# Performance work log

Measured on AMD Instinct MI355X. Metric: run time of the kernel, lower is better.

The kernel has to match this reference:

```python
import jax, jax.numpy as jnp
import numpy as np

NUM_FILTERS = 512
NUM_HEADS = 8
D_HEAD = NUM_FILTERS // NUM_HEADS


def setup_inputs() -> dict:
    key = jax.random.key(0)
    ks = jax.random.split(key, 11)
    B, W, H, F = 4, 48, 48, NUM_FILTERS
    s = 1.0 / np.sqrt(F)
    return {
        "query": jax.random.normal(ks[0], (B, W, H, F), jnp.float32),
        "value": jax.random.normal(ks[1], (B, W, H, F), jnp.float32),
        "keys": jax.random.normal(ks[2], (B, W, H, F), jnp.float32),
        "wq_w": jax.random.normal(ks[3], (F, F), jnp.float32) * s,
        "wq_b": jnp.zeros((F,), jnp.float32),
        "wk_w": jax.random.normal(ks[4], (F, F), jnp.float32) * s,
        "wk_b": jnp.zeros((F,), jnp.float32),
        "wv_w": jax.random.normal(ks[5], (F, F), jnp.float32) * s,
        "wv_b": jnp.zeros((F,), jnp.float32),
        "wo_w": jax.random.normal(ks[6], (F, F), jnp.float32) * s,
        "wo_b": jnp.zeros((F,), jnp.float32),
    }


def reference(query, value, keys, wq_w, wq_b, wk_w, wk_b, wv_w, wv_b, wo_w, wo_b):
    B, W, H, F = query.shape
    h, d = NUM_HEADS, D_HEAD
    # flatten spatial -> sequence, project, split heads: [B, h, S, d]
    def proj(x, w, b):
        x = x.reshape(B, -1, F) @ w + b
        return x.reshape(B, -1, h, d).transpose(0, 2, 1, 3)
    q = proj(query, wq_w, wq_b)
    k = proj(keys, wk_w, wk_b)
    v = proj(value, wv_w, wv_b)
    # scaled dot-product attention (mask=None path)
    logits = jnp.einsum('bhqd,bhkd->bhqk', q, k) / jnp.sqrt(jnp.asarray(d, q.dtype))
    attn = jax.nn.softmax(logits, axis=-1)            # [B, h, S, S]
    ctx = jnp.einsum('bhqk,bhkd->bhqd', attn, v)      # [B, h, S, d]
    ctx = ctx.transpose(0, 2, 1, 3).reshape(B, -1, F)  # [B, S, F]
    out = (ctx @ wo_w + wo_b).reshape(B, W, H, F)
    attn_weights = attn.reshape(B, h, W, H, -1)        # [B, h, W, H, S]
    return out, attn_weights
```

## Files before the change

kernel.cpp:

```cpp
#include <hip/hip_runtime.h>
#include <cstddef>

#define BB 4
#define SS 2304
#define FF 512
#define NH 8
#define DD 64
#define BSR (BB*SS)

typedef __attribute__((ext_vector_type(8))) short bf16x8;
typedef __attribute__((ext_vector_type(4))) float f32x4;
#define MFMA16(a,b,c) __builtin_amdgcn_mfma_f32_16x16x32_bf16((a),(b),(c),0,0,0)

__device__ __forceinline__ ushort f2bf_rne(float x) {
    uint u = __float_as_uint(x);
    uint r = u + 0x7fffu + ((u >> 16) & 1u);
    return (ushort)(r >> 16);
}
__device__ __forceinline__ float bfval(ushort h) {
    return __uint_as_float((uint)h << 16);
}

__global__ __launch_bounds__(256) void wtsplit_all(
    const float* __restrict__ w0, const float* __restrict__ w1,
    const float* __restrict__ w2, const float* __restrict__ w3,
    ushort* __restrict__ whi_all, ushort* __restrict__ wlo_all)
{
    __shared__ __align__(16) float tile[64][68];
    const int z = blockIdx.z;
    const float* w = (z == 0) ? w0 : (z == 1) ? w1 : (z == 2) ? w2 : w3;
    ushort* whi = whi_all + (size_t)z * FF * FF;
    ushort* wlo = wlo_all + (size_t)z * FF * FF;

    const int t  = threadIdx.x;
    const int kt = blockIdx.x;
    const int nt = blockIdx.y;
    {
        const int r  = t >> 2;
        const int cg = (t & 3) * 16;
        const float* src = w + (size_t)(kt * 64 + r) * FF + nt * 64 + cg;
        #pragma unroll
        for (int j = 0; j < 4; ++j)
            *(float4*)&tile[r][cg + 4 * j] = *(const float4*)(src + 4 * j);
    }
    __syncthreads();
    {
        const int n  = t >> 2;
        const int kg = (t & 3) * 16;
        union { ushort s[16]; uint4 q[2]; } H, L;
        #pragma unroll
        for (int j = 0; j < 16; ++j) {
            float x = tile[kg + j][n];
            ushort hh = f2bf_rne(x);
            H.s[j] = hh;
            L.s[j] = f2bf_rne(x - bfval(hh));
        }
        size_t off = (size_t)(nt * 64 + n) * FF + kt * 64 + kg;
        *(uint4*)(whi + off)     = H.q[0];
        *(uint4*)(whi + off + 8) = H.q[1];
        *(uint4*)(wlo + off)     = L.q[0];
        *(uint4*)(wlo + off + 8) = L.q[1];
    }
}

__global__ __launch_bounds__(256) void vtsplit_kernel(
    const float* __restrict__ v, ushort* __restrict__ vthi)
{
    __shared__ __align__(16) float tile[64][68];
    const int t  = threadIdx.x;
    const int st = blockIdx.x;
    const int bh = blockIdx.y;
    {
        const int r  = t >> 2;
        const int cg = (t & 3) * 16;
        const float* src = v + ((size_t)bh * SS + st * 64 + r) * DD + cg;
        #pragma unroll
        for (int j = 0; j < 4; ++j)
            *(float4*)&tile[r][cg + 4 * j] = *(const float4*)(src + 4 * j);
    }
    __syncthreads();
    {
        const int d  = t >> 2;
        const int sg = (t & 3) * 16;
        union { ushort s[16]; uint4 q[2]; } H;
        #pragma unroll
        for (int j = 0; j < 16; ++j) H.s[j] = f2bf_rne(tile[sg + j][d]);
        size_t off = ((size_t)bh * DD + d) * SS + st * 64 + sg;
        *(uint4*)(vthi + off)     = H.q[0];
        *(uint4*)(vthi + off + 8) = H.q[1];
    }
}

__global__ __launch_bounds__(256) void proj_qkv(
    const float* __restrict__ q_in, const float* __restrict__ k_in,
    const float* __restrict__ v_in, const ushort* __restrict__ whi_all,
    const ushort* __restrict__ wlo_all, const float* __restrict__ bq,
    const float* __restrict__ bk, const float* __restrict__ bv,
    ushort* __restrict__ qhi, ushort* __restrict__ qlo,
    ushort* __restrict__ khi, ushort* __restrict__ klo,
    float* __restrict__ vstage)
{
    const int z = blockIdx.z;
    const float* X = (z == 0) ? q_in : (z == 1) ? k_in : v_in;
    const ushort* wth = whi_all + (size_t)z * FF * FF;
    const ushort* wtl = wlo_all + (size_t)z * FF * FF;
    const float* bias = (z == 0) ? bq : (z == 1) ? bk : bv;

    const int t  = threadIdx.x, w = t >> 6, l = t & 63;
    const int ar = l & 15, kg = (l >> 4) * 8;
    const int i0 = blockIdx.x * 64, j0 = blockIdx.y * 128;
    const int arow = i0 + w * 16 + ar;

    f32x4 acc[8];
    #pragma unroll
    for (int nt = 0; nt < 8; ++nt) acc[nt] = (f32x4){0.f, 0.f, 0.f, 0.f};

    for (int kk = 0; kk < FF; kk += 32) {
        const float* xr = X + (size_t)arow * FF + kk + kg;
        float4 f0 = *(const float4*)xr;
        float4 f1 = *(const float4*)(xr + 4);
        ushort h0 = f2bf_rne(f0.x), h1 = f2bf_rne(f0.y), h2 = f2bf_rne(f0.z), h3 = f2bf_rne(f0.w);
        ushort h4 = f2bf_rne(f1.x), h5 = f2bf_rne(f1.y), h6 = f2bf_rne(f1.z), h7 = f2bf_rne(f1.w);
        union { uint u[4]; bf16x8 v; } ah, al;
        ah.u[0] = (uint)h0 | ((uint)h1 << 16);
        ah.u[1] = (uint)h2 | ((uint)h3 << 16);
        ah.u[2] = (uint)h4 | ((uint)h5 << 16);
        ah.u[3] = (uint)h6 | ((uint)h7 << 16);
        if (z < 2) {
            al.u[0] = (uint)f2bf_rne(f0.x - bfval(h0)) | ((uint)f2bf_rne(f0.y - bfval(h1)) << 16);
            al.u[1] = (uint)f2bf_rne(f0.z - bfval(h2)) | ((uint)f2bf_rne(f0.w - bfval(h3)) << 16);
            al.u[2] = (uint)f2bf_rne(f1.x - bfval(h4)) | ((uint)f2bf_rne(f1.y - bfval(h5)) << 16);
            al.u[3] = (uint)f2bf_rne(f1.z - bfval(h6)) | ((uint)f2bf_rne(f1.w - bfval(h7)) << 16);
        }
        #pragma unroll
        for (int nt = 0; nt < 8; ++nt) {
            const size_t wo = (size_t)(j0 + nt * 16 + ar) * FF + kk + kg;
            bf16x8 bh = *(const bf16x8*)(wth + wo);
            bf16x8 bl = *(const bf16x8*)(wtl + wo);
            acc[nt] = MFMA16(ah.v, bh, acc[nt]);
            acc[nt] = MFMA16(ah.v, bl, acc[nt]);
            if (z < 2) acc[nt] = MFMA16(al.v, bh, acc[nt]);
        }
    }

    const int bidx = i0 / SS;
    ushort* ohi = (z == 0) ? qhi : khi;
    ushort* olo = (z == 0) ? qlo : klo;
    #pragma unroll
    for (int nt = 0; nt < 8; ++nt) {
        const int col = j0 + nt * 16 + ar;
        const float bb = bias[col];
        #pragma unroll
        for (int r = 0; r < 4; ++r) {
            const int rowl = w * 16 + (l >> 4) * 4 + r;
            const float val = acc[nt][r] + bb;
            const int s = (i0 - bidx * SS) + rowl;
            const size_t o = (((size_t)bidx * NH + (col >> 6)) * SS + s) * DD + (col & 63);
            if (z == 2) {
                vstage[o] = val;
            } else {
                ushort hv = f2bf_rne(val);
                ohi[o] = hv;
                olo[o] = f2bf_rne(val - bfval(hv));
            }
        }
    }
}

__global__ __launch_bounds__(256) void proj_out(
    const float* __restrict__ X, const ushort* __restrict__ wth,
    const ushort* __restrict__ wtl, const float* __restrict__ bias,
    float* __restrict__ outf)
{
    const int t  = threadIdx.x, w = t >> 6, l = t & 63;
    const int ar = l & 15, kg = (l >> 4) * 8;
    const int i0 = blockIdx.x * 64, j0 = blockIdx.y * 128;
    const int arow = i0 + w * 16 + ar;

    f32x4 acc[8];
    #pragma unroll
    for (int nt = 0; nt < 8; ++nt) acc[nt] = (f32x4){0.f, 0.f, 0.f, 0.f};

    for (int kk = 0; kk < FF; kk += 32) {
        const float* xr = X + (size_t)arow * FF + kk + kg;
        float4 f0 = *(const float4*)xr;
        float4 f1 = *(const float4*)(xr + 4);
        union { uint u[4]; bf16x8 v; } ah;
        ah.u[0] = (uint)f2bf_rne(f0.x) | ((uint)f2bf_rne(f0.y) << 16);
        ah.u[1] = (uint)f2bf_rne(f0.z) | ((uint)f2bf_rne(f0.w) << 16);
        ah.u[2] = (uint)f2bf_rne(f1.x) | ((uint)f2bf_rne(f1.y) << 16);
        ah.u[3] = (uint)f2bf_rne(f1.z) | ((uint)f2bf_rne(f1.w) << 16);
        #pragma unroll
        for (int nt = 0; nt < 8; ++nt) {
            const size_t wo = (size_t)(j0 + nt * 16 + ar) * FF + kk + kg;
            bf16x8 bh = *(const bf16x8*)(wth + wo);
            bf16x8 bl = *(const bf16x8*)(wtl + wo);
            acc[nt] = MFMA16(ah.v, bh, acc[nt]);
            acc[nt] = MFMA16(ah.v, bl, acc[nt]);
        }
    }

    #pragma unroll
    for (int nt = 0; nt < 8; ++nt) {
        const int col = j0 + nt * 16 + ar;
        const float bb = bias[col];
        #pragma unroll
        for (int r = 0; r < 4; ++r) {
            const int rowl = w * 16 + (l >> 4) * 4 + r;
            outf[(size_t)(i0 + rowl) * FF + col] = acc[nt][r] + bb;
        }
    }
}

__global__ __launch_bounds__(512, 4) void fattn_kernel(
    const ushort* __restrict__ qhi, const ushort* __restrict__ qlo,
    const ushort* __restrict__ khi, const ushort* __restrict__ klo,
    const ushort* __restrict__ vthi,
    float* __restrict__ attn_out, float* __restrict__ ctx)
{
    __shared__ __align__(16) unsigned char smem[67584];
    ushort* KH0 = (ushort*)smem;
    ushort* KH1 = KH0 + 4096;
    ushort* KL0 = KH1 + 4096;
    ushort* KL1 = KL0 + 4096;
    ushort* VH0 = KL1 + 4096;
    ushort* VH1 = VH0 + 4096;
    float*  PT  = (float*)(VH1 + 4096);
    float*  redS = PT;

    const int t = threadIdx.x, w = t >> 6, l = t & 63;
    const int ar = l & 15, kgi = l >> 4;
    const int kg = kgi * 8;
    const int qs = w & 3, kh = w >> 2;

    const int xcd = blockIdx.x & 7;
    const int pos = blockIdx.x >> 3;
    const int bh  = xcd * 4 + (pos / 36);
    const int qt  = pos % 36;
    const int q0  = qt * 64;
    const int b   = bh >> 3, h = bh & 7;
    const size_t base = (size_t)bh * SS * DD;
    const float SC = 0.125f * 1.44269504f;

    const size_t qo = base + (size_t)(q0 + qs * 16 + ar) * DD + kg;
    const bf16x8 qh0 = *(const bf16x8*)(qhi + qo);
    const bf16x8 qh1 = *(const bf16x8*)(qhi + qo + 32);
    const bf16x8 ql0 = *(const bf16x8*)(qlo + qo);
    const bf16x8 ql1 = *(const bf16x8*)(qlo + qo + 32);

    const int srow = t >> 3, sc8 = t & 7;
    const int sidx = srow * 64 + ((sc8 ^ (srow & 7)) << 3);
    const ushort* khsrc = khi + base + srow * 64 + sc8 * 8;
    const ushort* klsrc = klo + base + srow * 64 + sc8 * 8;
    const ushort* vhsrc = vthi + ((size_t)bh * DD + srow) * SS + sc8 * 8;

    const int sw  = ar & 7;
    const int i00 = kh * 2048 + ar * 64;
    const int i01 = i00 + 1024;
    const int s00 = (kgi ^ sw) << 3;
    const int s01 = ((4 | kgi) ^ sw) << 3;
    const int svw = ((kh * 4 + kgi) ^ sw) << 3;

    float s_[4] = {0.f, 0.f, 0.f, 0.f};
    {
        uint4 rk = *(const uint4*)khsrc;
        *(uint4*)&KH0[sidx] = rk;
        __syncthreads();
        for (int kt = 0; kt < 36; ++kt) {
            if (kt < 35) rk = *(const uint4*)(khsrc + (size_t)(kt + 1) * 4096);
            const ushort* KC = (kt & 1) ? KH1 : KH0;
            bf16x8 b00 = *(const bf16x8*)&KC[i00 + s00];
            bf16x8 b01 = *(const bf16x8*)&KC[i00 + s01];
            bf16x8 b10 = *(const bf16x8*)&KC[i01 + s00];
            bf16x8 b11 = *(const bf16x8*)&KC[i01 + s01];
            f32x4 a0 = {0.f,0.f,0.f,0.f}, a1 = {0.f,0.f,0.f,0.f};
            __builtin_amdgcn_s_setprio(1);
            a0 = MFMA16(qh0, b00, a0); a1 = MFMA16(qh0, b10, a1);
            a0 = MFMA16(qh1, b01, a0); a1 = MFMA16(qh1, b11, a1);
            __builtin_amdgcn_s_setprio(0);
            #pragma unroll
            for (int r = 0; r < 4; ++r)
                s_[r] += exp2f(a0[r] * SC) + exp2f(a1[r] * SC);
            if (kt < 35) {
                ushort* KN = (kt & 1) ? KH0 : KH1;
                *(uint4*)&KN[sidx] = rk;
            }
            __syncthreads();
        }
    }
    #pragma unroll
    for (int off = 1; off <= 8; off <<= 1) {
        #pragma unroll
        for (int r = 0; r < 4; ++r) s_[r] += __shfl_xor(s_[r], off);
    }
    if (ar == 0) {
        #pragma unroll
        for (int r = 0; r < 4; ++r)
            redS[kh * 64 + qs * 16 + kgi * 4 + r] = s_[r];
    }
    __syncthreads();
    float inv[4];
    #pragma unroll
    for (int r = 0; r < 4; ++r) {
        const int idx = qs * 16 + kgi * 4 + r;
        inv[r] = 1.0f / (redS[idx] + redS[64 + idx]);
    }

    float* PTw = PT + w * 576;
    float* asto = attn_out + ((size_t)bh * SS + q0 + qs * 16 + (l >> 2)) * SS
                + kh * 32 + (l & 3) * 8;

    f32x4 acc[4];
    #pragma unroll
    for (int nt = 0; nt < 4; ++nt) acc[nt] = (f32x4){0.f, 0.f, 0.f, 0.f};

    {
        uint4 a = *(const uint4*)khsrc;
        uint4 bq = *(const uint4*)klsrc;
        uint4 c = *(const uint4*)vhsrc;
        *(uint4*)&KH0[sidx] = a;
        *(uint4*)&KL0[sidx] = bq;
        *(uint4*)&VH0[sidx] = c;
    }
    __syncthreads();

    for (int kt = 0; kt < 36; ++kt) {
        uint4 rkh, rkl, rvh;
        if (kt < 35) {
            rkh = *(const uint4*)(khsrc + (size_t)(kt + 1) * 4096);
            rkl = *(const uint4*)(klsrc + (size_t)(kt + 1) * 4096);
            rvh = *(const uint4*)(vhsrc + (size_t)(kt + 1) * 64);
        }
        const ushort* KHc = (kt & 1) ? KH1 : KH0;
        const ushort* KLc = (kt & 1) ? KL1 : KL0;
        const ushort* VHc = (kt & 1) ? VH1 : VH0;

        bf16x8 bh00 = *(const bf16x8*)&KHc[i00 + s00];
        bf16x8 bh01 = *(const bf16x8*)&KHc[i00 + s01];
        bf16x8 bl00 = *(const bf16x8*)&KLc[i00 + s00];
        bf16x8 bl01 = *(const bf16x8*)&KLc[i00 + s01];
        bf16x8 bh10 = *(const bf16x8*)&KHc[i01 + s00];
        bf16x8 bh11 = *(const bf16x8*)&KHc[i01 + s01];
        bf16x8 bl10 = *(const bf16x8*)&KLc[i01 + s00];
        bf16x8 bl11 = *(const bf16x8*)&KLc[i01 + s01];
        f32x4 a0 = {0.f,0.f,0.f,0.f}, a1 = {0.f,0.f,0.f,0.f};
        __builtin_amdgcn_s_setprio(1);
        a0 = MFMA16(qh0, bh00, a0); a1 = MFMA16(qh0, bh10, a1);
        a0 = MFMA16(qh0, bl00, a0); a1 = MFMA16(qh0, bl10, a1);
        a0 = MFMA16(ql0, bh00, a0); a1 = MFMA16(ql0, bh10, a1);
        a0 = MFMA16(qh1, bh01, a0); a1 = MFMA16(qh1, bh11, a1);
        a0 = MFMA16(qh1, bl01, a0); a1 = MFMA16(qh1, bl11, a1);
        a0 = MFMA16(ql1, bh01, a0); a1 = MFMA16(ql1, bh11, a1);
        __builtin_amdgcn_s_setprio(0);

        #pragma unroll
        for (int r = 0; r < 4; ++r) {
            const int row = kgi * 4 + r;
            float p0 = exp2f(a0[r] * SC) * inv[r];
            float p1 = exp2f(a1[r] * SC) * inv[r];
            PTw[row * 36 + ar]      = p0;
            PTw[row * 36 + 16 + ar] = p1;
        }

        {
            const float* psr = PTw + (l >> 2) * 36 + (l & 3) * 8;
            f32x4 sv0 = *(const f32x4*)psr;
            f32x4 sv1 = *(const f32x4*)(psr + 4);
            f32x4* dst = (f32x4*)(asto + (size_t)kt * 64);
            __builtin_nontemporal_store(sv0, dst);
            __builtin_nontemporal_store(sv1, dst + 1);
        }

        {
            const float* par = PTw + ar * 36 + kg;
            f32x4 pf0 = *(const f32x4*)par;
            f32x4 pf1 = *(const f32x4*)(par + 4);
            union { uint u[4]; bf16x8 v; } pah, pal;
            ushort hh[8]; float rr[8];
            #pragma unroll
            for (int j = 0; j < 4; ++j) {
                hh[j]     = f2bf_rne(pf0[j]); rr[j]     = pf0[j] - bfval(hh[j]);
                hh[4 + j] = f2bf_rne(pf1[j]); rr[4 + j] = pf1[j] - bfval(hh[4 + j]);
            }
            #pragma unroll
            for (int j = 0; j < 4; ++j) {
                pah.u[j] = (uint)hh[2*j] | ((uint)hh[2*j+1] << 16);
                pal.u[j] = (uint)f2bf_rne(rr[2*j]) | ((uint)f2bf_rne(rr[2*j+1]) << 16);
            }
            __builtin_amdgcn_s_setprio(1);
            #pragma unroll
            for (int nt = 0; nt < 4; ++nt) {
                const int vfi = (nt * 16 + ar) * 64 + svw;
                bf16x8 vh = *(const bf16x8*)&VHc[vfi];
                acc[nt] = MFMA16(pah.v, vh, acc[nt]);
                acc[nt] = MFMA16(pal.v, vh, acc[nt]);
            }
            __builtin_amdgcn_s_setprio(0);
        }

        if (kt < 35) {
            ushort* KHN = (kt & 1) ? KH0 : KH1;
            ushort* KLN = (kt & 1) ? KL0 : KL1;
            ushort* VHN = (kt & 1) ? VH0 : VH1;
            *(uint4*)&KHN[sidx] = rkh;
            *(uint4*)&KLN[sidx] = rkl;
            *(uint4*)&VHN[sidx] = rvh;
        }
        __syncthreads();
    }

    float* SCR = (float*)smem;
    #pragma unroll
    for (int nt = 0; nt < 4; ++nt) {
        #pragma unroll
        for (int r = 0; r < 4; ++r)
            SCR[w * 1088 + (kgi * 4 + r) * 68 + nt * 16 + ar] = acc[nt][r];
    }
    __syncthreads();
    {
        const int rrow = t >> 3;
        const int dg   = (t & 7) * 8;
        const int rqs  = rrow >> 4, rl = rrow & 15;
        const float* s0p = SCR + rqs * 1088 + rl * 68 + dg;
        const float* s1p = s0p + 4 * 1088;
        f32x4 o0, o1;
        #pragma unroll
        for (int j = 0; j < 4; ++j) o0[j] = s0p[j] + s1p[j];
        #pragma unroll
        for (int j = 0; j < 4; ++j) o1[j] = s0p[4 + j] + s1p[4 + j];
        float* cdst = ctx + ((size_t)b * SS + q0 + rrow) * FF + h * DD + dg;
        *(f32x4*)cdst = o0;
        *(f32x4*)(cdst + 4) = o1;
    }
}

extern "C" void kernel_launch(void* const* d_in, const int* in_sizes, int n_in,
                              void* d_out, int out_size, void* d_ws, size_t ws_size,
                              hipStream_t stream) {
    (void)in_sizes; (void)n_in; (void)out_size; (void)ws_size;
    const float* query = (const float*)d_in[0];
    const float* value = (const float*)d_in[1];
    const float* keys  = (const float*)d_in[2];
    const float* wq_w  = (const float*)d_in[3];
    const float* wq_b  = (const float*)d_in[4];
    const float* wk_w  = (const float*)d_in[5];
    const float* wk_b  = (const float*)d_in[6];
    const float* wv_w  = (const float*)d_in[7];
    const float* wv_b  = (const float*)d_in[8];
    const float* wo_w  = (const float*)d_in[9];
    const float* wo_b  = (const float*)d_in[10];

    float* out  = (float*)d_out;
    float* attn = out + (size_t)BB * SS * FF;

    const size_t NQ = (size_t)BB * NH * SS * DD;
    ushort* qhi    = (ushort*)d_ws;
    ushort* qlo    = qhi + NQ;
    ushort* khi    = qlo + NQ;
    ushort* klo    = khi + NQ;
    ushort* vthi   = klo + NQ;
    float*  vstage = (float*)(vthi + NQ);
    ushort* wthi   = (ushort*)(vstage + NQ);
    ushort* wtlo   = wthi + (size_t)4 * FF * FF;

    dim3 gwt(FF / 64, FF / 64, 4);
    dim3 gqkv(BSR / 64, FF / 128, 3);
    dim3 gproj(BSR / 64, FF / 128);
    dim3 gvt(SS / 64, BB * NH);

    wtsplit_all<<<gwt, 256, 0, stream>>>(wq_w, wk_w, wv_w, wo_w, wthi, wtlo);
    proj_qkv<<<gqkv, 256, 0, stream>>>(query, keys, value, wthi, wtlo,
                                       wq_b, wk_b, wv_b,
                                       qhi, qlo, khi, klo, vstage);
    vtsplit_kernel<<<gvt, 256, 0, stream>>>(vstage, vthi);

    fattn_kernel<<<36 * 32, 512, 0, stream>>>(qhi, qlo, khi, klo, vthi,
                                              attn, vstage);

    proj_out<<<gproj, 256, 0, stream>>>(vstage, wthi + (size_t)3 * FF * FF,
                                        wtlo + (size_t)3 * FF * FF, wo_b, out);
}
```

Baseline: 640.3 us.

## Fuse V transpose into projection epilogue and use packed bf16 conversions

Removes the separate vtsplit kernel by having proj_qkv write V already transposed to bf16 via a shared-memory tile. The Q/K epilogue is also staged through LDS so hi/lo outputs go out as coalesced 16-byte stores. Manual bf16 rounding is replaced by the hardware v_cvt_pk_bf16_f32 instruction throughout. The softmax normalisation is folded into the exp2 argument as a log-domain offset. Together these cut a kernel launch and an fp32 round trip, at the cost of extra LDS use and barriers in the projection epilogue.

New measurement: 603.4 us (median of 2 runs). 1.06x faster.

```diff
diff --git a/kernel.cpp b/kernel.cpp
--- a/kernel.cpp
+++ b/kernel.cpp
@@ -20,6 +20,13 @@
 __device__ __forceinline__ float bfval(ushort h) {
     return __uint_as_float((uint)h << 16);
 }
+__device__ __forceinline__ uint cvt_pk_bf16(float a, float b) {
+    uint r;
+    asm("v_cvt_pk_bf16_f32 %0, %1, %2" : "=v"(r) : "v"(a), "v"(b));
+    return r;
+}
+__device__ __forceinline__ float lo16val(uint p) { return __uint_as_float(p << 16); }
+__device__ __forceinline__ float hi16val(uint p) { return __uint_as_float(p & 0xffff0000u); }
 
 __global__ __launch_bounds__(256) void wtsplit_all(
     const float* __restrict__ w0, const float* __restrict__ w1,
@@ -47,47 +54,20 @@
     {
         const int n  = t >> 2;
         const int kg = (t & 3) * 16;
-        union { ushort s[16]; uint4 q[2]; } H, L;
-        #pragma unroll
-        for (int j = 0; j < 16; ++j) {
-            float x = tile[kg + j][n];
-            ushort hh = f2bf_rne(x);
-            H.s[j] = hh;
-            L.s[j] = f2bf_rne(x - bfval(hh));
+        uint H[8], L[8];
+        #pragma unroll
+        for (int j = 0; j < 8; ++j) {
+            float x0 = tile[kg + 2 * j][n];
+            float x1 = tile[kg + 2 * j + 1][n];
+            uint hp = cvt_pk_bf16(x0, x1);
+            H[j] = hp;
+            L[j] = cvt_pk_bf16(x0 - lo16val(hp), x1 - hi16val(hp));
         }
         size_t off = (size_t)(nt * 64 + n) * FF + kt * 64 + kg;
-        *(uint4*)(whi + off)     = H.q[0];
-        *(uint4*)(whi + off + 8) = H.q[1];
-        *(uint4*)(wlo + off)     = L.q[0];
-        *(uint4*)(wlo + off + 8) = L.q[1];
-    }
-}
-
-__global__ __launch_bounds__(256) void vtsplit_kernel(
-    const float* __restrict__ v, ushort* __restrict__ vthi)
-{
-    __shared__ __align__(16) float tile[64][68];
-    const int t  = threadIdx.x;
-    const int st = blockIdx.x;
-    const int bh = blockIdx.y;
-    {
-        const int r  = t >> 2;
-        const int cg = (t & 3) * 16;
-        const float* src = v + ((size_t)bh * SS + st * 64 + r) * DD + cg;
-        #pragma unroll
-        for (int j = 0; j < 4; ++j)
-            *(float4*)&tile[r][cg + 4 * j] = *(const float4*)(src + 4 * j);
-    }
-    __syncthreads();
-    {
-        const int d  = t >> 2;
-        const int sg = (t & 3) * 16;
-        union { ushort s[16]; uint4 q[2]; } H;
-        #pragma unroll
-        for (int j = 0; j < 16; ++j) H.s[j] = f2bf_rne(tile[sg + j][d]);
-        size_t off = ((size_t)bh * DD + d) * SS + st * 64 + sg;
-        *(uint4*)(vthi + off)     = H.q[0];
-        *(uint4*)(vthi + off + 8) = H.q[1];
+        *(uint4*)(whi + off)     = make_uint4(H[0], H[1], H[2], H[3]);
+        *(uint4*)(whi + off + 8) = make_uint4(H[4], H[5], H[6], H[7]);
+        *(uint4*)(wlo + off)     = make_uint4(L[0], L[1], L[2], L[3]);
+        *(uint4*)(wlo + off + 8) = make_uint4(L[4], L[5], L[6], L[7]);
     }
 }
 
@@ -98,8 +78,10 @@
     const float* __restrict__ bk, const float* __restrict__ bv,
     ushort* __restrict__ qhi, ushort* __restrict__ qlo,
     ushort* __restrict__ khi, ushort* __restrict__ klo,
-    float* __restrict__ vstage)
+    ushort* __restrict__ vthi)
 {
+    __shared__ __align__(16) ushort TL[9216];
+
     const int z = blockIdx.z;
     const float* X = (z == 0) ? q_in : (z == 1) ? k_in : v_in;
     const ushort* wth = whi_all + (size_t)z * FF * FF;
@@ -119,18 +101,16 @@
         const float* xr = X + (size_t)arow * FF + kk + kg;
         float4 f0 = *(const float4*)xr;
         float4 f1 = *(const float4*)(xr + 4);
-        ushort h0 = f2bf_rne(f0.x), h1 = f2bf_rne(f0.y), h2 = f2bf_rne(f0.z), h3 = f2bf_rne(f0.w);
-        ushort h4 = f2bf_rne(f1.x), h5 = f2bf_rne(f1.y), h6 = f2bf_rne(f1.z), h7 = f2bf_rne(f1.w);
         union { uint u[4]; bf16x8 v; } ah, al;
-        ah.u[0] = (uint)h0 | ((uint)h1 << 16);
-        ah.u[1] = (uint)h2 | ((uint)h3 << 16);
-        ah.u[2] = (uint)h4 | ((uint)h5 << 16);
-        ah.u[3] = (uint)h6 | ((uint)h7 << 16);
+        ah.u[0] = cvt_pk_bf16(f0.x, f0.y);
+        ah.u[1] = cvt_pk_bf16(f0.z, f0.w);
+        ah.u[2] = cvt_pk_bf16(f1.x, f1.y);
+        ah.u[3] = cvt_pk_bf16(f1.z, f1.w);
         if (z < 2) {
-            al.u[0] = (uint)f2bf_rne(f0.x - bfval(h0)) | ((uint)f2bf_rne(f0.y - bfval(h1)) << 16);
-            al.u[1] = (uint)f2bf_rne(f0.z - bfval(h2)) | ((uint)f2bf_rne(f0.w - bfval(h3)) << 16);
-            al.u[2] = (uint)f2bf_rne(f1.x - bfval(h4)) | ((uint)f2bf_rne(f1.y - bfval(h5)) << 16);
-            al.u[3] = (uint)f2bf_rne(f1.z - bfval(h6)) | ((uint)f2bf_rne(f1.w - bfval(h7)) << 16);
+            al.u[0] = cvt_pk_bf16(f0.x - lo16val(ah.u[0]), f0.y - hi16val(ah.u[0]));
+            al.u[1] = cvt_pk_bf16(f0.z - lo16val(ah.u[1]), f0.w - hi16val(ah.u[1]));
+            al.u[2] = cvt_pk_bf16(f1.x - lo16val(ah.u[2]), f1.y - hi16val(ah.u[2]));
+            al.u[3] = cvt_pk_bf16(f1.z - lo16val(ah.u[3]), f1.w - hi16val(ah.u[3]));
         }
         #pragma unroll
         for (int nt = 0; nt < 8; ++nt) {
@@ -144,25 +124,66 @@
     }
 
     const int bidx = i0 / SS;
-    ushort* ohi = (z == 0) ? qhi : khi;
-    ushort* olo = (z == 0) ? qlo : klo;
-    #pragma unroll
-    for (int nt = 0; nt < 8; ++nt) {
-        const int col = j0 + nt * 16 + ar;
-        const float bb = bias[col];
-        #pragma unroll
-        for (int r = 0; r < 4; ++r) {
-            const int rowl = w * 16 + (l >> 4) * 4 + r;
-            const float val = acc[nt][r] + bb;
-            const int s = (i0 - bidx * SS) + rowl;
-            const size_t o = (((size_t)bidx * NH + (col >> 6)) * SS + s) * DD + (col & 63);
-            if (z == 2) {
-                vstage[o] = val;
-            } else {
-                ushort hv = f2bf_rne(val);
-                ohi[o] = hv;
-                olo[o] = f2bf_rne(val - bfval(hv));
+    const int s0b  = i0 - bidx * SS;
+    const int rowl = w * 16 + ((l >> 4) << 2);
+
+    if (z == 2) {
+        #pragma unroll
+        for (int nt = 0; nt < 8; ++nt) {
+            const float bb = bias[j0 + nt * 16 + ar];
+            #pragma unroll
+            for (int r = 0; r < 4; ++r)
+                TL[(nt * 16 + ar) * 72 + rowl + r] = f2bf_rne(acc[nt][r] + bb);
+        }
+        __syncthreads();
+        const int d = t >> 1, hf = t & 1;
+        const ushort* src = &TL[d * 72 + hf * 32];
+        const size_t o = (((size_t)bidx * NH + ((j0 + d) >> 6)) * DD + (d & 63)) * SS
+                       + s0b + hf * 32;
+        *(uint4*)(vthi + o)      = *(const uint4*)(src);
+        *(uint4*)(vthi + o + 8)  = *(const uint4*)(src + 8);
+        *(uint4*)(vthi + o + 16) = *(const uint4*)(src + 16);
+        *(uint4*)(vthi + o + 24) = *(const uint4*)(src + 24);
+    } else {
+        ushort* ohi = (z == 0) ? qhi : khi;
+        ushort* olo = (z == 0) ? qlo : klo;
+        const int rowf = t >> 2, qd = t & 3;
+        const int colg = j0 + qd * 32;
+        const size_t o = (((size_t)bidx * NH + (colg >> 6)) * SS + s0b + rowf) * DD
+                       + (colg & 63);
+        #pragma unroll
+        for (int nt = 0; nt < 8; ++nt) {
+            const float bb = bias[j0 + nt * 16 + ar];
+            #pragma unroll
+            for (int r = 0; r < 4; ++r)
+                TL[(rowl + r) * 136 + nt * 16 + ar] = f2bf_rne(acc[nt][r] + bb);
+        }
+        __syncthreads();
+        {
+            const ushort* src = &TL[rowf * 136 + qd * 32];
+            *(uint4*)(ohi + o)      = *(const uint4*)(src);
+            *(uint4*)(ohi + o + 8)  = *(const uint4*)(src + 8);
+            *(uint4*)(ohi + o + 16) = *(const uint4*)(src + 16);
+            *(uint4*)(ohi + o + 24) = *(const uint4*)(src + 24);
+        }
+        __syncthreads();
+        #pragma unroll
+        for (int nt = 0; nt < 8; ++nt) {
+            const float bb = bias[j0 + nt * 16 + ar];
+            #pragma unroll
+            for (int r = 0; r < 4; ++r) {
+                const float val = acc[nt][r] + bb;
+                const ushort hv = f2bf_rne(val);
+                TL[(rowl + r) * 136 + nt * 16 + ar] = f2bf_rne(val - bfval(hv));
             }
+        }
+        __syncthreads();
+        {
+            const ushort* src = &TL[rowf * 136 + qd * 32];
+            *(uint4*)(olo + o)      = *(const uint4*)(src);
+            *(uint4*)(olo + o + 8)  = *(const uint4*)(src + 8);
+            *(uint4*)(olo + o + 16) = *(const uint4*)(src + 16);
+            *(uint4*)(olo + o + 24) = *(const uint4*)(src + 24);
         }
     }
 }
@@ -186,10 +207,10 @@
         float4 f0 = *(const float4*)xr;
         float4 f1 = *(const float4*)(xr + 4);
         union { uint u[4]; bf16x8 v; } ah;
-        ah.u[0] = (uint)f2bf_rne(f0.x) | ((uint)f2bf_rne(f0.y) << 16);
-        ah.u[1] = (uint)f2bf_rne(f0.z) | ((uint)f2bf_rne(f0.w) << 16);
-        ah.u[2] = (uint)f2bf_rne(f1.x) | ((uint)f2bf_rne(f1.y) << 16);
-        ah.u[3] = (uint)f2bf_rne(f1.z) | ((uint)f2bf_rne(f1.w) << 16);
+        ah.u[0] = cvt_pk_bf16(f0.x, f0.y);
+        ah.u[1] = cvt_pk_bf16(f0.z, f0.w);
+        ah.u[2] = cvt_pk_bf16(f1.x, f1.y);
+        ah.u[3] = cvt_pk_bf16(f1.z, f1.w);
         #pragma unroll
         for (int nt = 0; nt < 8; ++nt) {
             const size_t wo = (size_t)(j0 + nt * 16 + ar) * FF + kk + kg;
@@ -299,11 +320,11 @@
             redS[kh * 64 + qs * 16 + kgi * 4 + r] = s_[r];
     }
     __syncthreads();
-    float inv[4];
+    float linv[4];
     #pragma unroll
     for (int r = 0; r < 4; ++r) {
         const int idx = qs * 16 + kgi * 4 + r;
-        inv[r] = 1.0f / (redS[idx] + redS[64 + idx]);
+        linv[r] = -__log2f(redS[idx] + redS[64 + idx]);
     }
 
     float* PTw = PT + w * 576;
@@ -356,8 +377,8 @@
         #pragma unroll
         for (int r = 0; r < 4; ++r) {
             const int row = kgi * 4 + r;
-            float p0 = exp2f(a0[r] * SC) * inv[r];
-            float p1 = exp2f(a1[r] * SC) * inv[r];
+            float p0 = exp2f(fmaf(a0[r], SC, linv[r]));
+            float p1 = exp2f(fmaf(a1[r], SC, linv[r]));
             PTw[row * 36 + ar]      = p0;
             PTw[row * 36 + 16 + ar] = p1;
         }
@@ -376,17 +397,14 @@
             f32x4 pf0 = *(const f32x4*)par;
             f32x4 pf1 = *(const f32x4*)(par + 4);
             union { uint u[4]; bf16x8 v; } pah, pal;
-            ushort hh[8]; float rr[8];
-            #pragma unroll
-            for (int j = 0; j < 4; ++j) {
-                hh[j]     = f2bf_rne(pf0[j]); rr[j]     = pf0[j] - bfval(hh[j]);
-                hh[4 + j] = f2bf_rne(pf1[j]); rr[4 + j] = pf1[j] - bfval(hh[4 + j]);
-            }
-            #pragma unroll
-            for (int j = 0; j < 4; ++j) {
-                pah.u[j] = (uint)hh[2*j] | ((uint)hh[2*j+1] << 16);
-                pal.u[j] = (uint)f2bf_rne(rr[2*j]) | ((uint)f2bf_rne(rr[2*j+1]) << 16);
-            }
+            pah.u[0] = cvt_pk_bf16(pf0[0], pf0[1]);
+            pah.u[1] = cvt_pk_bf16(pf0[2], pf0[3]);
+            pah.u[2] = cvt_pk_bf16(pf1[0], pf1[1]);
+            pah.u[3] = cvt_pk_bf16(pf1[2], pf1[3]);
+            pal.u[0] = cvt_pk_bf16(pf0[0] - lo16val(pah.u[0]), pf0[1] - hi16val(pah.u[0]));
+            pal.u[1] = cvt_pk_bf16(pf0[2] - lo16val(pah.u[1]), pf0[3] - hi16val(pah.u[1]));
+            pal.u[2] = cvt_pk_bf16(pf1[0] - lo16val(pah.u[2]), pf1[1] - hi16val(pah.u[2]));
+            pal.u[3] = cvt_pk_bf16(pf1[2] - lo16val(pah.u[3]), pf1[3] - hi16val(pah.u[3]));
             __builtin_amdgcn_s_setprio(1);
             #pragma unroll
             for (int nt = 0; nt < 4; ++nt) {
@@ -466,13 +484,11 @@
     dim3 gwt(FF / 64, FF / 64, 4);
     dim3 gqkv(BSR / 64, FF / 128, 3);
     dim3 gproj(BSR / 64, FF / 128);
-    dim3 gvt(SS / 64, BB * NH);
 
     wtsplit_all<<<gwt, 256, 0, stream>>>(wq_w, wk_w, wv_w, wo_w, wthi, wtlo);
     proj_qkv<<<gqkv, 256, 0, stream>>>(query, keys, value, wthi, wtlo,
                                        wq_b, wk_b, wv_b,
-                                       qhi, qlo, khi, klo, vstage);
-    vtsplit_kernel<<<gvt, 256, 0, stream>>>(vstage, vthi);
+                                       qhi, qlo, khi, klo, vthi);
 
     fattn_kernel<<<36 * 32, 512, 0, stream>>>(qhi, qlo, khi, klo, vthi,
                                               attn, vstage);
```
